# Kernel optimization log

Hardware: AMD Instinct MI355X
Metric: run time of the kernel (lower is better)

The kernel has to match this reference:

```python
import jax, jax.numpy as jnp
import numpy as np

B, C, H, W = 8, 1024, 64, 64

def setup_inputs() -> dict:
    key = jax.random.key(0)
    k1, k2, k3, k4 = jax.random.split(key, 4)
    return {
        "prev_key": jax.random.normal(k1, (B, C, H, W), dtype=jnp.float32),
        "prev_value": jax.random.normal(k2, (B, C, H, W), dtype=jnp.float32),
        "curr_key": jax.random.normal(k3, (B, C, H, W), dtype=jnp.float32),
        "curr_value": jax.random.normal(k4, (B, C, H, W), dtype=jnp.float32),
    }


def _get_affinity(mk, qk):
    # mk, qk: [B, CK, N]  (N = H*W)
    CK = mk.shape[1]
    a_sq = jnp.sum(mk * mk, axis=1)[:, :, None]          # [B, N, 1]
    ab = jnp.einsum('bcn,bcm->bnm', mk, qk)              # [B, N, N]
    affinity = (2.0 * ab - a_sq) / jnp.sqrt(jnp.asarray(CK, mk.dtype))
    # softmax over memory positions (dim 1), numerically stable
    return jax.nn.softmax(affinity, axis=1)              # [B, N, N]


def reference(prev_key, prev_value, curr_key, curr_value):
    b, ck, h, w = prev_key.shape
    n = h * w
    mk = prev_key.reshape(b, ck, n)
    qk = curr_key.reshape(b, ck, n)
    affinity = _get_affinity(mk, qk)                     # [B, N, N]
    cv = prev_value.shape[1]
    mo = prev_value.reshape(b, cv, n)                    # [B, CV, N]
    mem = jnp.einsum('bcn,bnm->bcm', mo, affinity)       # [B, CV, N]
    mem = mem.reshape(b, cv, h, w)
    return jnp.concatenate([mem, curr_value], axis=1)    # [B, 2*CV, H, W]
```

## Files before the change

### kernel.cpp

```cpp
#include <hip/hip_runtime.h>
#include <hip/hip_bf16.h>

#define BATCH 8
#define CH    1024
#define NN    4096

typedef __attribute__((ext_vector_type(8))) short bf16x8;
typedef __attribute__((ext_vector_type(4))) float f32x4;
using bf16 = __hip_bfloat16;

struct bhalf4 { bf16 x, y, z, w; };

__device__ __forceinline__ unsigned short f2bfu(float f) {
  bf16 h = __float2bfloat16(f);
  return *reinterpret_cast<unsigned short*>(&h);
}

template <bool ASQ>
__global__ __launch_bounds__(256) void transpose_cast_v(
    const float* __restrict__ in_all, bf16* __restrict__ out_all,
    float* __restrict__ asq_all) {
  int bz = blockIdx.z;
  const float* in = in_all + (size_t)bz * CH * NN;
  bf16* out = out_all + (size_t)bz * NN * CH;

  __shared__ float tile[64][65];
  __shared__ float sqb[16][64];

  int n0 = blockIdx.x * 64;
  int c0 = blockIdx.y * 64;
  int t = threadIdx.x;
  int nc = t & 15;
  int cr = t >> 4;

  float4 sq4 = make_float4(0.f, 0.f, 0.f, 0.f);
#pragma unroll
  for (int i = 0; i < 4; ++i) {
    int c = cr + i * 16;
    float4 v = *(const float4*)(in + (size_t)(c0 + c) * NN + n0 + nc * 4);
    tile[c][nc * 4 + 0] = v.x;
    tile[c][nc * 4 + 1] = v.y;
    tile[c][nc * 4 + 2] = v.z;
    tile[c][nc * 4 + 3] = v.w;
    if (ASQ) {
      sq4.x += v.x * v.x; sq4.y += v.y * v.y;
      sq4.z += v.z * v.z; sq4.w += v.w * v.w;
    }
  }
  if (ASQ) {
    sqb[cr][nc * 4 + 0] = sq4.x;
    sqb[cr][nc * 4 + 1] = sq4.y;
    sqb[cr][nc * 4 + 2] = sq4.z;
    sqb[cr][nc * 4 + 3] = sq4.w;
  }
  __syncthreads();
  if (ASQ && t < 64) {
    float s = 0.f;
#pragma unroll
    for (int i = 0; i < 16; ++i) s += sqb[i][t];
    atomicAdd(&asq_all[(size_t)bz * NN + n0 + t], s);
  }
  int cchunk = t & 7;
  int nb = t >> 3;
#pragma unroll
  for (int p = 0; p < 2; ++p) {
    int n = nb + p * 32;
    bf16x8 o;
#pragma unroll
    for (int j = 0; j < 8; ++j)
      o[j] = (short)f2bfu(tile[cchunk * 8 + j][n]);
    *(bf16x8*)(out + (size_t)(n0 + n) * CH + c0 + cchunk * 8) = o;
  }
}

__global__ __launch_bounds__(256) void convert_cast(
    const float4* __restrict__ in, bhalf4* __restrict__ out) {
  size_t i = (size_t)blockIdx.x * 256 + threadIdx.x;
  float4 v = in[i];
  bhalf4 o;
  o.x = __float2bfloat16(v.x);
  o.y = __float2bfloat16(v.y);
  o.z = __float2bfloat16(v.z);
  o.w = __float2bfloat16(v.w);
  out[i] = o;
}

#define BARR() __builtin_amdgcn_s_barrier()
#define PRIO(x) __builtin_amdgcn_s_setprio(x)
#define LDS_FENCE() do {                                      \
    asm volatile("s_waitcnt lgkmcnt(0)" ::: "memory");        \
    __builtin_amdgcn_sched_barrier(0);                        \
  } while (0)
#define MEM_FENCE() do {                                      \
    asm volatile("" ::: "memory");                            \
    __builtin_amdgcn_sched_barrier(0);                        \
  } while (0)

__device__ __forceinline__ void gload16(const bf16* g, bf16* l) {
  __builtin_amdgcn_global_load_lds(
      (const __attribute__((address_space(1))) void*)g,
      (__attribute__((address_space(3))) void*)l, 16, 0, 0);
}

template <int K, int MODE, int TM, int TN>
__global__ __launch_bounds__(256, 2) void gemm_s3(
    const bf16* __restrict__ Aall, const bf16* __restrict__ Ball,
    bf16* __restrict__ Pall, float* __restrict__ Oall,
    const float* __restrict__ asq_all, float* __restrict__ rsum_all) {
  constexpr int NT = K / 32;
  constexpr int TPB = TM * TN;
  constexpr int NWG = TPB * BATCH;
  constexpr int GRP = (TM < 8) ? TM : 8;

  int lid = blockIdx.x;
  int swz = (lid & 7) * (NWG >> 3) + (lid >> 3);
  int bz  = swz / TPB;
  int rem = swz - bz * TPB;
  int g  = rem / (GRP * TN);
  int r2 = rem - g * (GRP * TN);
  int bx = r2 / GRP;
  int by = g * GRP + (r2 & (GRP - 1));

  const bf16* Ab = Aall + (size_t)bz * TM * 256 * K + (size_t)(by * 256) * K;
  const bf16* Bb = Ball + (size_t)bz * TN * 128 * K + (size_t)(bx * 128) * K;

  __shared__ bf16 As[3][256 * 32];
  __shared__ bf16 Bs[3][128 * 32];
  bf16* const AsB = &As[0][0];
  bf16* const BsB = &Bs[0][0];

  int tid = threadIdx.x;
  int wv = tid >> 6, lane = tid & 63;
  int fl = lane & 15, quad = lane >> 4;
  int wr = wv >> 1, wc = wv & 1;

  int rA0 = tid >> 2,           cA0 = (tid & 3) ^ ((rA0 >> 1) & 3);
  int rA1 = (256 + tid) >> 2,   cA1 = ((256 + tid) & 3) ^ ((rA1 >> 1) & 3);
  int rA2 = (512 + tid) >> 2,   cA2 = ((512 + tid) & 3) ^ ((rA2 >> 1) & 3);
  int rA3 = (768 + tid) >> 2,   cA3 = ((768 + tid) & 3) ^ ((rA3 >> 1) & 3);
  const bf16* gA0 = Ab + (size_t)rA0 * K + cA0 * 8;
  const bf16* gA1 = Ab + (size_t)rA1 * K + cA1 * 8;
  const bf16* gA2 = Ab + (size_t)rA2 * K + cA2 * 8;
  const bf16* gA3 = Ab + (size_t)rA3 * K + cA3 * 8;
  const bf16* gB0 = Bb + (size_t)rA0 * K + cA0 * 8;
  const bf16* gB1 = Bb + (size_t)rA1 * K + cA1 * 8;
  int lsu = wv * 512;

  int kq = (quad ^ ((fl >> 1) & 3)) * 8;
  int aoff = (wr * 128 + fl) * 32 + kq;
  int boff = (wc * 64 + fl) * 32 + kq;

  f32x4 acc[8][4] = {};

#define STAGE2(SB) do {                                                       \
    bf16* da = AsB + (SB) * 8192;                                             \
    bf16* db = BsB + (SB) * 4096;                                             \
    gload16(gA0, da + lsu);        gload16(gA1, da + 2048 + lsu);             \
    gload16(gA2, da + 4096 + lsu); gload16(gA3, da + 6144 + lsu);             \
    gload16(gB0, db + lsu);        gload16(gB1, db + 2048 + lsu);             \
    gA0 += 32; gA1 += 32; gA2 += 32; gA3 += 32; gB0 += 32; gB1 += 32;         \
  } while (0)

  STAGE2(0);
  STAGE2(1);
  asm volatile("s_waitcnt vmcnt(6)" ::: "memory");
  BARR();

  int cb = 0, sb = 2;
  for (int t = 0; t < NT; ++t) {
    const bf16* Ac = AsB + cb * 8192;
    const bf16* Bc = BsB + cb * 4096;
    bf16x8 aF[8], bF[4];
#pragma unroll
    for (int mi = 0; mi < 8; ++mi)
      aF[mi] = *(const bf16x8*)(Ac + aoff + mi * 512);
#pragma unroll
    for (int nj = 0; nj < 4; ++nj)
      bF[nj] = *(const bf16x8*)(Bc + boff + nj * 512);

    if (t + 2 < NT) STAGE2(sb);

    BARR();
    asm volatile("s_waitcnt lgkmcnt(0)" ::: "memory");
    __builtin_amdgcn_sched_barrier(0);
    PRIO(1);
#pragma unroll
    for (int mi = 0; mi < 8; ++mi)
#pragma unroll
      for (int nj = 0; nj < 4; ++nj)
        acc[mi][nj] = __builtin_amdgcn_mfma_f32_16x16x32_bf16(
            aF[mi], bF[nj], acc[mi][nj], 0, 0, 0);
    PRIO(0);
    if (t + 2 < NT) {
      asm volatile("s_waitcnt vmcnt(6)" ::: "memory");
    } else {
      asm volatile("s_waitcnt vmcnt(0)" ::: "memory");
    }
    BARR();

    cb = (cb == 2) ? 0 : cb + 1;
    sb = (sb == 2) ? 0 : sb + 1;
  }
#undef STAGE2

  __syncthreads();

  int colbase = bx * 128 + wc * 64;
  int rowg0 = by * 256 + wr * 128;

  if constexpr (MODE == 0) {
    const float* asq = asq_all + (size_t)bz * NN;
    float* rsum = rsum_all + (size_t)bz * NN;
    bf16* P = Pall + (size_t)bz * NN * NN;
    short* scr = (short*)AsB + wv * 1024;

    float aq[4];
#pragma unroll
    for (int nj = 0; nj < 4; ++nj) aq[nj] = asq[colbase + nj * 16 + fl];

    float rs[8][4];
#pragma unroll
    for (int mi = 0; mi < 8; ++mi)
#pragma unroll
      for (int r = 0; r < 4; ++r) rs[mi][r] = 0.f;

#pragma unroll
    for (int mi = 0; mi < 8; ++mi) {
#pragma unroll
      for (int nj = 0; nj < 4; ++nj)
#pragma unroll
        for (int r = 0; r < 4; ++r) {
          int row = (quad << 2) + r;
          float e = __expf((2.f * acc[mi][nj][r] - aq[nj]) * 0.03125f);
          rs[mi][r] += e;
          int chunk = (nj * 2 + (fl >> 3)) ^ (row & 7);
          scr[row * 64 + chunk * 8 + (fl & 7)] = (short)f2bfu(e);
        }
      LDS_FENCE();
#pragma unroll
      for (int p = 0; p < 2; ++p) {
        int row = (p << 3) + (lane >> 3);
        int c = lane & 7;
        int chunk = c ^ (row & 7);
        bf16x8 v = *(const bf16x8*)(scr + row * 64 + chunk * 8);
        *(bf16x8*)(P + (size_t)(rowg0 + mi * 16 + row) * NN + colbase + c * 8) = v;
      }
      MEM_FENCE();
    }
#pragma unroll
    for (int mi = 0; mi < 8; ++mi)
#pragma unroll
      for (int r = 0; r < 4; ++r) {
        float v = rs[mi][r];
        v += __shfl_xor(v, 1);
        v += __shfl_xor(v, 2);
        v += __shfl_xor(v, 4);
        v += __shfl_xor(v, 8);
        if (fl == 0)
          atomicAdd(&rsum[rowg0 + mi * 16 + (quad << 2) + r], v);
      }
  } else {
    float* Co = Oall + (size_t)bz * 2 * CH * NN;
    const float* rsum = rsum_all + (size_t)bz * NN;
    float* scr = (float*)AsB + wv * 1024;

    float inv[4];
#pragma unroll
    for (int nj = 0; nj < 4; ++nj) inv[nj] = 1.f / rsum[colbase + nj * 16 + fl];

#pragma unroll
    for (int mi = 0; mi < 8; ++mi) {
#pragma unroll
      for (int nj = 0; nj < 4; ++nj)
#pragma unroll
        for (int r = 0; r < 4; ++r) {
          int row = (quad << 2) + r;
          int chunk = (nj * 4 + (fl >> 2)) ^ (row & 15);
          scr[row * 64 + chunk * 4 + (fl & 3)] = acc[mi][nj][r] * inv[nj];
        }
      LDS_FENCE();
#pragma unroll
      for (int p = 0; p < 4; ++p) {
        int row = (p << 2) + (lane >> 4);
        int c = lane & 15;
        int chunk = c ^ (row & 15);
        f32x4 v = *(const f32x4*)(scr + row * 64 + chunk * 4);
        *(f32x4*)(Co + (size_t)(rowg0 + mi * 16 + row) * NN + colbase + c * 4) = v;
      }
      MEM_FENCE();
    }
  }
}

__global__ __launch_bounds__(256) void copy_curr(
    const float4* __restrict__ src, float4* __restrict__ dst) {
  size_t idx = (size_t)blockIdx.x * 256 + threadIdx.x;
  size_t b = idx >> 20;
  size_t r = idx & 1048575;
  dst[b * 2097152 + 1048576 + r] = src[idx];
}

extern "C" void kernel_launch(void* const* d_in, const int* in_sizes, int n_in,
                              void* d_out, int out_size, void* d_ws, size_t ws_size,
                              hipStream_t stream) {
  const float* prev_key   = (const float*)d_in[0];
  const float* prev_value = (const float*)d_in[1];
  const float* curr_key   = (const float*)d_in[2];
  const float* curr_value = (const float*)d_in[3];
  float* out = (float*)d_out;

  char* ws = (char*)d_ws;
  bf16* P     = (bf16*)(ws);
  bf16* mk_t  = (bf16*)(ws + 268435456u);
  bf16* qk_t  = (bf16*)(ws + 335544320u);
  bf16* mo_b  = (bf16*)(ws + 402653184u);
  float* a_sq = (float*)(ws + 469762048u);
  float* rsum = a_sq + (size_t)BATCH * NN;

  hipMemsetAsync(a_sq, 0, 2ull * BATCH * NN * sizeof(float), stream);

  transpose_cast_v<true><<<dim3(NN / 64, CH / 64, BATCH), 256, 0, stream>>>(
      prev_key, mk_t, a_sq);
  transpose_cast_v<false><<<dim3(NN / 64, CH / 64, BATCH), 256, 0, stream>>>(
      curr_key, qk_t, nullptr);
  convert_cast<<<(size_t)BATCH * CH * NN / 4 / 256, 256, 0, stream>>>(
      (const float4*)prev_value, (bhalf4*)mo_b);

  gemm_s3<CH, 0, 16, 32><<<dim3(16 * 32 * BATCH), dim3(256), 0, stream>>>(
      qk_t, mk_t, P, nullptr, a_sq, rsum);

  gemm_s3<NN, 1, 4, 32><<<dim3(4 * 32 * BATCH), dim3(256), 0, stream>>>(
      mo_b, P, nullptr, out, nullptr, rsum);

  copy_curr<<<(size_t)BATCH * CH * NN / 4 / 256, 256, 0, stream>>>(
      (const float4*)curr_value, (float4*)out);
}
```

Before: 1.187 ms.

## Pre-pack A operands into MFMA fragment layout and load directly to registers

The A operands (query keys and memory values) are now written by the preprocessing kernels in a blocked fragment-order layout, so the GEMM waves load their A fragments straight from global memory into registers with double buffering instead of staging them through LDS. Only B is staged in LDS, and the tile shape changes to 512x64 per workgroup with each wave owning 128 rows. This removes LDS traffic and barrier pressure for A, at the cost of more register-file usage, per-wave global loads of A with no sharing across waves, and a less coalesced B reuse pattern. The copy of curr_value is also moved ahead of the GEMMs.

After: 1.283 ms. 1.08x slower.

```diff
diff --git a/kernel.cpp b/kernel.cpp
--- a/kernel.cpp
+++ b/kernel.cpp
@@ -16,8 +16,7 @@
   return *reinterpret_cast<unsigned short*>(&h);
 }
 
-template <bool ASQ>
-__global__ __launch_bounds__(256) void transpose_cast_v(
+__global__ __launch_bounds__(256) void transpose_cast_asq(
     const float* __restrict__ in_all, bf16* __restrict__ out_all,
     float* __restrict__ asq_all) {
   int bz = blockIdx.z;
@@ -42,19 +41,15 @@
     tile[c][nc * 4 + 1] = v.y;
     tile[c][nc * 4 + 2] = v.z;
     tile[c][nc * 4 + 3] = v.w;
-    if (ASQ) {
-      sq4.x += v.x * v.x; sq4.y += v.y * v.y;
-      sq4.z += v.z * v.z; sq4.w += v.w * v.w;
-    }
-  }
-  if (ASQ) {
-    sqb[cr][nc * 4 + 0] = sq4.x;
-    sqb[cr][nc * 4 + 1] = sq4.y;
-    sqb[cr][nc * 4 + 2] = sq4.z;
-    sqb[cr][nc * 4 + 3] = sq4.w;
-  }
+    sq4.x += v.x * v.x; sq4.y += v.y * v.y;
+    sq4.z += v.z * v.z; sq4.w += v.w * v.w;
+  }
+  sqb[cr][nc * 4 + 0] = sq4.x;
+  sqb[cr][nc * 4 + 1] = sq4.y;
+  sqb[cr][nc * 4 + 2] = sq4.z;
+  sqb[cr][nc * 4 + 3] = sq4.w;
   __syncthreads();
-  if (ASQ && t < 64) {
+  if (t < 64) {
     float s = 0.f;
 #pragma unroll
     for (int i = 0; i < 16; ++i) s += sqb[i][t];
@@ -73,16 +68,85 @@
   }
 }
 
-__global__ __launch_bounds__(256) void convert_cast(
-    const float4* __restrict__ in, bhalf4* __restrict__ out) {
-  size_t i = (size_t)blockIdx.x * 256 + threadIdx.x;
-  float4 v = in[i];
-  bhalf4 o;
-  o.x = __float2bfloat16(v.x);
-  o.y = __float2bfloat16(v.y);
-  o.z = __float2bfloat16(v.z);
-  o.w = __float2bfloat16(v.w);
-  out[i] = o;
+__global__ __launch_bounds__(256) void transpose_pack(
+    const float* __restrict__ in_all, bf16* __restrict__ out_all) {
+  int bz = blockIdx.z;
+  const float* in = in_all + (size_t)bz * CH * NN;
+  bf16* out = out_all + (size_t)bz * NN * CH;
+
+  __shared__ float tile[64][65];
+  int n0 = blockIdx.x * 64;
+  int c0 = blockIdx.y * 64;
+  int t = threadIdx.x;
+  int nc = t & 15;
+  int cr = t >> 4;
+#pragma unroll
+  for (int i = 0; i < 4; ++i) {
+    int c = cr + i * 16;
+    float4 v = *(const float4*)(in + (size_t)(c0 + c) * NN + n0 + nc * 4);
+    tile[c][nc * 4 + 0] = v.x;
+    tile[c][nc * 4 + 1] = v.y;
+    tile[c][nc * 4 + 2] = v.z;
+    tile[c][nc * 4 + 3] = v.w;
+  }
+  __syncthreads();
+  constexpr int NKB = CH / 32;
+#pragma unroll
+  for (int p = 0; p < 2; ++p) {
+    int q = p * 256 + t;
+    int s = q >> 6, l = q & 63;
+    int rbl = s & 3, kbl = s >> 2;
+    int cl = kbl * 32 + (l >> 4) * 8;
+    int nl = rbl * 16 + (l & 15);
+    bf16x8 o;
+#pragma unroll
+    for (int j = 0; j < 8; ++j) o[j] = (short)f2bfu(tile[cl + j][nl]);
+    size_t rb = (size_t)(n0 >> 4) + rbl;
+    size_t kb = (size_t)(c0 >> 5) + kbl;
+    *(bf16x8*)(out + (rb * NKB + kb) * 512 + l * 8) = o;
+  }
+}
+
+__global__ __launch_bounds__(256) void convert_pack(
+    const float* __restrict__ in_all, bf16* __restrict__ out_all) {
+  int bz = blockIdx.z;
+  const float* in = in_all + (size_t)bz * CH * NN;
+  bf16* out = out_all + (size_t)bz * CH * NN;
+
+  __shared__ float tile[16][132];
+  int m0 = blockIdx.x * 128;
+  int c0 = blockIdx.y * 16;
+  int t = threadIdx.x;
+  int mq = t & 31;
+  int cr = t >> 5;
+#pragma unroll
+  for (int i = 0; i < 2; ++i) {
+    int c = cr + i * 8;
+    float4 v = *(const float4*)(in + (size_t)(c0 + c) * NN + m0 + mq * 4);
+    tile[c][mq * 4 + 0] = v.x;
+    tile[c][mq * 4 + 1] = v.y;
+    tile[c][mq * 4 + 2] = v.z;
+    tile[c][mq * 4 + 3] = v.w;
+  }
+  __syncthreads();
+  constexpr int NKB = NN / 32;
+  int s = t >> 6, l = t & 63;
+  int cl = l & 15;
+  int ml = s * 32 + (l >> 4) * 8;
+  bf16x8 o;
+#pragma unroll
+  for (int j = 0; j < 8; ++j) o[j] = (short)f2bfu(tile[cl][ml + j]);
+  size_t rb = (size_t)(c0 >> 4);
+  size_t kb = (size_t)(m0 >> 5) + s;
+  *(bf16x8*)(out + (rb * NKB + kb) * 512 + l * 8) = o;
+}
+
+__global__ __launch_bounds__(256) void copy_curr(
+    const float4* __restrict__ src, float4* __restrict__ dst) {
+  size_t idx = (size_t)blockIdx.x * 256 + threadIdx.x;
+  size_t b = idx >> 20;
+  size_t r = idx & 1048575;
+  dst[b * 2097152 + 1048576 + r] = src[idx];
 }
 
 #define BARR() __builtin_amdgcn_s_barrier()
@@ -96,123 +160,125 @@
     __builtin_amdgcn_sched_barrier(0);                        \
   } while (0)
 
-__device__ __forceinline__ void gload16(const bf16* g, bf16* l) {
-  __builtin_amdgcn_global_load_lds(
-      (const __attribute__((address_space(1))) void*)g,
-      (__attribute__((address_space(3))) void*)l, 16, 0, 0);
-}
-
-template <int K, int MODE, int TM, int TN>
-__global__ __launch_bounds__(256, 2) void gemm_s3(
-    const bf16* __restrict__ Aall, const bf16* __restrict__ Ball,
+template <int K, int MODE, int TM>
+__global__ __launch_bounds__(256, 2) void gemm_ad(
+    const bf16* __restrict__ Apk, const bf16* __restrict__ Ball,
     bf16* __restrict__ Pall, float* __restrict__ Oall,
     const float* __restrict__ asq_all, float* __restrict__ rsum_all) {
   constexpr int NT = K / 32;
-  constexpr int TPB = TM * TN;
-  constexpr int NWG = TPB * BATCH;
+  constexpr int NKB = K / 32;
+  constexpr int TN = NN / 64;
+  constexpr int NWG = TM * TN * BATCH;
   constexpr int GRP = (TM < 8) ? TM : 8;
 
   int lid = blockIdx.x;
   int swz = (lid & 7) * (NWG >> 3) + (lid >> 3);
-  int bz  = swz / TPB;
-  int rem = swz - bz * TPB;
+  int bz  = swz / (TM * TN);
+  int rem = swz - bz * (TM * TN);
   int g  = rem / (GRP * TN);
   int r2 = rem - g * (GRP * TN);
   int bx = r2 / GRP;
   int by = g * GRP + (r2 & (GRP - 1));
 
-  const bf16* Ab = Aall + (size_t)bz * TM * 256 * K + (size_t)(by * 256) * K;
-  const bf16* Bb = Ball + (size_t)bz * TN * 128 * K + (size_t)(bx * 128) * K;
-
-  __shared__ bf16 As[3][256 * 32];
-  __shared__ bf16 Bs[3][128 * 32];
-  bf16* const AsB = &As[0][0];
-  bf16* const BsB = &Bs[0][0];
+  const bf16* Bb = Ball + (size_t)bz * NN * (size_t)K + (size_t)(bx * 64) * K;
+
+  __shared__ bf16 Bs[8192];
 
   int tid = threadIdx.x;
   int wv = tid >> 6, lane = tid & 63;
   int fl = lane & 15, quad = lane >> 4;
-  int wr = wv >> 1, wc = wv & 1;
-
-  int rA0 = tid >> 2,           cA0 = (tid & 3) ^ ((rA0 >> 1) & 3);
-  int rA1 = (256 + tid) >> 2,   cA1 = ((256 + tid) & 3) ^ ((rA1 >> 1) & 3);
-  int rA2 = (512 + tid) >> 2,   cA2 = ((512 + tid) & 3) ^ ((rA2 >> 1) & 3);
-  int rA3 = (768 + tid) >> 2,   cA3 = ((768 + tid) & 3) ^ ((rA3 >> 1) & 3);
-  const bf16* gA0 = Ab + (size_t)rA0 * K + cA0 * 8;
-  const bf16* gA1 = Ab + (size_t)rA1 * K + cA1 * 8;
-  const bf16* gA2 = Ab + (size_t)rA2 * K + cA2 * 8;
-  const bf16* gA3 = Ab + (size_t)rA3 * K + cA3 * 8;
-  const bf16* gB0 = Bb + (size_t)rA0 * K + cA0 * 8;
-  const bf16* gB1 = Bb + (size_t)rA1 * K + cA1 * 8;
-  int lsu = wv * 512;
+
+  int rS = tid >> 2;
+  int cS = (tid & 3) ^ ((rS >> 1) & 3);
+  const bf16* gB = Bb + (size_t)rS * K + cS * 8;
+  int lsB = wv * 512;
 
   int kq = (quad ^ ((fl >> 1) & 3)) * 8;
-  int aoff = (wr * 128 + fl) * 32 + kq;
-  int boff = (wc * 64 + fl) * 32 + kq;
+  int boff = fl * 32 + kq;
+
+  int rb0 = by * 32 + wv * 8;
+  const bf16* aB = Apk + (size_t)bz * ((size_t)TM * 512) * K +
+                   (size_t)rb0 * NKB * 512 + lane * 8;
 
   f32x4 acc[8][4] = {};
-
-#define STAGE2(SB) do {                                                       \
-    bf16* da = AsB + (SB) * 8192;                                             \
-    bf16* db = BsB + (SB) * 4096;                                             \
-    gload16(gA0, da + lsu);        gload16(gA1, da + 2048 + lsu);             \
-    gload16(gA2, da + 4096 + lsu); gload16(gA3, da + 6144 + lsu);             \
-    gload16(gB0, db + lsu);        gload16(gB1, db + 2048 + lsu);             \
-    gA0 += 32; gA1 += 32; gA2 += 32; gA3 += 32; gB0 += 32; gB1 += 32;         \
-  } while (0)
-
-  STAGE2(0);
-  STAGE2(1);
-  asm volatile("s_waitcnt vmcnt(6)" ::: "memory");
+  bf16x8 a0[8], a1[8], bF[4];
+
+#define LOADA(DST) do {                                                       \
+    _Pragma("unroll")                                                         \
+    for (int mi_ = 0; mi_ < 8; ++mi_)                                         \
+      DST[mi_] = *(const bf16x8*)(aB + (size_t)mi_ * (NKB * 512));            \
+    aB += 512;                                                                \
+  } while (0)
+#define STAGEB(SB) do {                                                       \
+    __builtin_amdgcn_global_load_lds(                                         \
+        (const __attribute__((address_space(1))) void*)gB,                    \
+        (__attribute__((address_space(3))) void*)(Bs + (SB) * 2048 + lsB),    \
+        16, 0, 0);                                                            \
+    gB += 32;                                                                 \
+  } while (0)
+#define RDB(CB) do {                                                          \
+    _Pragma("unroll")                                                         \
+    for (int nj_ = 0; nj_ < 4; ++nj_)                                         \
+      bF[nj_] = *(const bf16x8*)(Bs + (CB) * 2048 + boff + nj_ * 512);        \
+  } while (0)
+#define MFMA8(AS) do {                                                        \
+    PRIO(1);                                                                  \
+    _Pragma("unroll")                                                         \
+    for (int mi_ = 0; mi_ < 8; ++mi_)                                         \
+      _Pragma("unroll")                                                       \
+      for (int nj_ = 0; nj_ < 4; ++nj_)                                       \
+        acc[mi_][nj_] = __builtin_amdgcn_mfma_f32_16x16x32_bf16(              \
+            AS[mi_], bF[nj_], acc[mi_][nj_], 0, 0, 0);                        \
+    PRIO(0);                                                                  \
+  } while (0)
+
+  STAGEB(0);
+  STAGEB(1);
+  LOADA(a0);
+  asm volatile("s_waitcnt vmcnt(0)" ::: "memory");
   BARR();
 
   int cb = 0, sb = 2;
-  for (int t = 0; t < NT; ++t) {
-    const bf16* Ac = AsB + cb * 8192;
-    const bf16* Bc = BsB + cb * 4096;
-    bf16x8 aF[8], bF[4];
-#pragma unroll
-    for (int mi = 0; mi < 8; ++mi)
-      aF[mi] = *(const bf16x8*)(Ac + aoff + mi * 512);
-#pragma unroll
-    for (int nj = 0; nj < 4; ++nj)
-      bF[nj] = *(const bf16x8*)(Bc + boff + nj * 512);
-
-    if (t + 2 < NT) STAGE2(sb);
-
-    BARR();
+  for (int t = 0; t < NT; t += 2) {
+    RDB(cb);
+    LOADA(a1);
+    if (t + 2 < NT) STAGEB(sb);
     asm volatile("s_waitcnt lgkmcnt(0)" ::: "memory");
     __builtin_amdgcn_sched_barrier(0);
-    PRIO(1);
-#pragma unroll
-    for (int mi = 0; mi < 8; ++mi)
-#pragma unroll
-      for (int nj = 0; nj < 4; ++nj)
-        acc[mi][nj] = __builtin_amdgcn_mfma_f32_16x16x32_bf16(
-            aF[mi], bF[nj], acc[mi][nj], 0, 0, 0);
-    PRIO(0);
-    if (t + 2 < NT) {
-      asm volatile("s_waitcnt vmcnt(6)" ::: "memory");
-    } else {
-      asm volatile("s_waitcnt vmcnt(0)" ::: "memory");
-    }
+    MFMA8(a0);
+    if (t + 2 < NT) { asm volatile("s_waitcnt vmcnt(1)" ::: "memory"); }
+    else            { asm volatile("s_waitcnt vmcnt(0)" ::: "memory"); }
     BARR();
-
     cb = (cb == 2) ? 0 : cb + 1;
     sb = (sb == 2) ? 0 : sb + 1;
-  }
-#undef STAGE2
+
+    RDB(cb);
+    if (t + 2 < NT) LOADA(a0);
+    if (t + 3 < NT) STAGEB(sb);
+    asm volatile("s_waitcnt lgkmcnt(0)" ::: "memory");
+    __builtin_amdgcn_sched_barrier(0);
+    MFMA8(a1);
+    if (t + 3 < NT) { asm volatile("s_waitcnt vmcnt(1)" ::: "memory"); }
+    else            { asm volatile("s_waitcnt vmcnt(0)" ::: "memory"); }
+    BARR();
+    cb = (cb == 2) ? 0 : cb + 1;
+    sb = (sb == 2) ? 0 : sb + 1;
+  }
+#undef LOADA
+#undef STAGEB
+#undef RDB
+#undef MFMA8
 
   __syncthreads();
 
-  int colbase = bx * 128 + wc * 64;
-  int rowg0 = by * 256 + wr * 128;
+  int colbase = bx * 64;
+  int rowg0 = by * 512 + wv * 128;
 
   if constexpr (MODE == 0) {
     const float* asq = asq_all + (size_t)bz * NN;
     float* rsum = rsum_all + (size_t)bz * NN;
     bf16* P = Pall + (size_t)bz * NN * NN;
-    short* scr = (short*)AsB + wv * 1024;
+    short* scr = (short*)Bs + wv * 1024;
 
     float aq[4];
 #pragma unroll
@@ -262,7 +328,7 @@
   } else {
     float* Co = Oall + (size_t)bz * 2 * CH * NN;
     const float* rsum = rsum_all + (size_t)bz * NN;
-    float* scr = (float*)AsB + wv * 1024;
+    float* scr = (float*)Bs + wv * 1024;
 
     float inv[4];
 #pragma unroll
@@ -292,14 +358,6 @@
   }
 }
 
-__global__ __launch_bounds__(256) void copy_curr(
-    const float4* __restrict__ src, float4* __restrict__ dst) {
-  size_t idx = (size_t)blockIdx.x * 256 + threadIdx.x;
-  size_t b = idx >> 20;
-  size_t r = idx & 1048575;
-  dst[b * 2097152 + 1048576 + r] = src[idx];
-}
-
 extern "C" void kernel_launch(void* const* d_in, const int* in_sizes, int n_in,
                               void* d_out, int out_size, void* d_ws, size_t ws_size,
                               hipStream_t stream) {
@@ -312,26 +370,25 @@
   char* ws = (char*)d_ws;
   bf16* P     = (bf16*)(ws);
   bf16* mk_t  = (bf16*)(ws + 268435456u);
-  bf16* qk_t  = (bf16*)(ws + 335544320u);
-  bf16* mo_b  = (bf16*)(ws + 402653184u);
+  bf16* qk_p  = (bf16*)(ws + 335544320u);
+  bf16* mo_p  = (bf16*)(ws + 402653184u);
   float* a_sq = (float*)(ws + 469762048u);
   float* rsum = a_sq + (size_t)BATCH * NN;
 
   hipMemsetAsync(a_sq, 0, 2ull * BATCH * NN * sizeof(float), stream);
 
-  transpose_cast_v<true><<<dim3(NN / 64, CH / 64, BATCH), 256, 0, stream>>>(
+  transpose_cast_asq<<<dim3(NN / 64, CH / 64, BATCH), 256, 0, stream>>>(
       prev_key, mk_t, a_sq);
-  transpose_cast_v<false><<<dim3(NN / 64, CH / 64, BATCH), 256, 0, stream>>>(
-      curr_key, qk_t, nullptr);
-  convert_cast<<<(size_t)BATCH * CH * NN / 4 / 256, 256, 0, stream>>>(
-      (const float4*)prev_value, (bhalf4*)mo_b);
-
-  gemm_s3<CH, 0, 16, 32><<<dim3(16 * 32 * BATCH), dim3(256), 0, stream>>>(
-      qk_t, mk_t, P, nullptr, a_sq, rsum);
-
-  gemm_s3<NN, 1, 4, 32><<<dim3(4 * 32 * BATCH), dim3(256), 0, stream>>>(
-      mo_b, P, nullptr, out, nullptr, rsum);
-
+  transpose_pack<<<dim3(NN / 64, CH / 64, BATCH), 256, 0, stream>>>(
+      curr_key, qk_p);
+  convert_pack<<<dim3(NN / 128, CH / 16, BATCH), 256, 0, stream>>>(
+      prev_value, mo_p);
   copy_curr<<<(size_t)BATCH * CH * NN / 4 / 256, 256, 0, stream>>>(
       (const float4*)curr_value, (float4*)out);
-}
+
+  gemm_ad<CH, 0, 8><<<dim3(8 * 64 * BATCH), dim3(256), 0, stream>>>(
+      qk_p, mk_t, P, nullptr, a_sq, rsum);
+
+  gemm_ad<NN, 1, 2><<<dim3(2 * 64 * BATCH), dim3(256), 0, stream>>>(
+      mo_p, P, nullptr, out, nullptr, rsum);
+}
```

## Fold value cast and curr copy into first GEMM launch as interleaved blocks

Applied to the files above, without the earlier changes.

Removes the separate convert_cast and copy_curr launches. Their memory-bound work now runs as extra workgroups, every fifth block, inside the first GEMM grid, which grows to 5120 blocks. Each side block grid-strides over 64 float4 chunks. The aim is to overlap these bandwidth-bound copies with the compute-bound GEMM and save two launches, at the risk of the copy blocks competing with GEMM tiles for bandwidth and CU slots.

Result: slower. 1.216 ms (+2.5%).

```diff
diff --git a/kernel.cpp b/kernel.cpp
--- a/kernel.cpp
+++ b/kernel.cpp
@@ -73,18 +73,6 @@
   }
 }
 
-__global__ __launch_bounds__(256) void convert_cast(
-    const float4* __restrict__ in, bhalf4* __restrict__ out) {
-  size_t i = (size_t)blockIdx.x * 256 + threadIdx.x;
-  float4 v = in[i];
-  bhalf4 o;
-  o.x = __float2bfloat16(v.x);
-  o.y = __float2bfloat16(v.y);
-  o.z = __float2bfloat16(v.z);
-  o.w = __float2bfloat16(v.w);
-  out[i] = o;
-}
-
 #define BARR() __builtin_amdgcn_s_barrier()
 #define PRIO(x) __builtin_amdgcn_s_setprio(x)
 #define LDS_FENCE() do {                                      \
@@ -102,17 +90,53 @@
       (__attribute__((address_space(3))) void*)l, 16, 0, 0);
 }
 
-template <int K, int MODE, int TM, int TN>
+template <int K, int MODE, int TM, int TN, bool FUSE>
 __global__ __launch_bounds__(256, 2) void gemm_s3(
     const bf16* __restrict__ Aall, const bf16* __restrict__ Ball,
     bf16* __restrict__ Pall, float* __restrict__ Oall,
-    const float* __restrict__ asq_all, float* __restrict__ rsum_all) {
+    const float* __restrict__ asq_all, float* __restrict__ rsum_all,
+    const float4* __restrict__ pv_src, bhalf4* __restrict__ mo_dst,
+    const float4* __restrict__ cv_src, float4* __restrict__ out_dst) {
   constexpr int NT = K / 32;
   constexpr int TPB = TM * TN;
   constexpr int NWG = TPB * BATCH;
   constexpr int GRP = (TM < 8) ? TM : 8;
 
-  int lid = blockIdx.x;
+  int lid;
+  if constexpr (FUSE) {
+    int bid = blockIdx.x;
+    if ((bid % 5) == 4) {
+      int mb = bid / 5;
+      int tid = threadIdx.x;
+      if (mb < 512) {
+        size_t idx = (size_t)mb * 256 + tid;
+#pragma unroll 4
+        for (int i = 0; i < 64; ++i, idx += 131072) {
+          float4 v = pv_src[idx];
+          bhalf4 o;
+          o.x = __float2bfloat16(v.x);
+          o.y = __float2bfloat16(v.y);
+          o.z = __float2bfloat16(v.z);
+          o.w = __float2bfloat16(v.w);
+          mo_dst[idx] = o;
+        }
+      } else {
+        size_t idx = (size_t)(mb - 512) * 256 + tid;
+#pragma unroll 4
+        for (int i = 0; i < 64; ++i, idx += 131072) {
+          float4 v = cv_src[idx];
+          size_t b = idx >> 20;
+          size_t r = idx & 1048575;
+          out_dst[b * 2097152 + 1048576 + r] = v;
+        }
+      }
+      return;
+    }
+    lid = bid - bid / 5;
+  } else {
+    lid = blockIdx.x;
+  }
+
   int swz = (lid & 7) * (NWG >> 3) + (lid >> 3);
   int bz  = swz / TPB;
   int rem = swz - bz * TPB;
@@ -292,14 +316,6 @@
   }
 }
 
-__global__ __launch_bounds__(256) void copy_curr(
-    const float4* __restrict__ src, float4* __restrict__ dst) {
-  size_t idx = (size_t)blockIdx.x * 256 + threadIdx.x;
-  size_t b = idx >> 20;
-  size_t r = idx & 1048575;
-  dst[b * 2097152 + 1048576 + r] = src[idx];
-}
-
 extern "C" void kernel_launch(void* const* d_in, const int* in_sizes, int n_in,
                               void* d_out, int out_size, void* d_ws, size_t ws_size,
                               hipStream_t stream) {
@@ -323,15 +339,13 @@
       prev_key, mk_t, a_sq);
   transpose_cast_v<false><<<dim3(NN / 64, CH / 64, BATCH), 256, 0, stream>>>(
       curr_key, qk_t, nullptr);
-  convert_cast<<<(size_t)BATCH * CH * NN / 4 / 256, 256, 0, stream>>>(
-      (const float4*)prev_value, (bhalf4*)mo_b);
-
-  gemm_s3<CH, 0, 16, 32><<<dim3(16 * 32 * BATCH), dim3(256), 0, stream>>>(
-      qk_t, mk_t, P, nullptr, a_sq, rsum);
-
-  gemm_s3<NN, 1, 4, 32><<<dim3(4 * 32 * BATCH), dim3(256), 0, stream>>>(
-      mo_b, P, nullptr, out, nullptr, rsum);
-
-  copy_curr<<<(size_t)BATCH * CH * NN / 4 / 256, 256, 0, stream>>>(
+
+  gemm_s3<CH, 0, 16, 32, true><<<dim3(5120), dim3(256), 0, stream>>>(
+      qk_t, mk_t, P, nullptr, a_sq, rsum,
+      (const float4*)prev_value, (bhalf4*)mo_b,
       (const float4*)curr_value, (float4*)out);
-}
+
+  gemm_s3<NN, 1, 4, 32, false><<<dim3(4 * 32 * BATCH), dim3(256), 0, stream>>>(
+      mo_b, P, nullptr, out, nullptr, rsum,
+      nullptr, nullptr, nullptr, nullptr);
+}
```
